# Performance work log

Hardware: AMD Instinct MI355X
Metric: run time of the kernel (lower is better)

The kernel has to match this reference:

```python
import jax, jax.numpy as jnp
import numpy as np

N = 50000      # nodes
E = 800000     # edges (before self-loops)
DIN = 146      # input feature dim
D = 128        # hidden/out dim
G = 64         # graphs in batch
L = 4          # number of GCNConv layers (len(hidden_dims[1:]) + 1)
NC = 10        # classes
EPS = 1e-5     # BatchNorm eps


def setup_inputs() -> dict:
    key = jax.random.key(0)
    ks = jax.random.split(key, 12)
    x = jax.random.normal(ks[0], (N, DIN), jnp.float32)
    edge_index = jax.random.randint(ks[1], (2, E), 0, N, dtype=jnp.int64)
    batch = jnp.sort(jax.random.randint(ks[2], (N,), 0, G, dtype=jnp.int64))

    def lin(k, shape, fan_in):
        return (jax.random.normal(k, shape, jnp.float32) / np.sqrt(fan_in)).astype(jnp.float32)

    W_emb = lin(ks[3], (DIN, D), DIN)
    b_emb = jnp.zeros((D,), jnp.float32)
    W_gcn = lin(ks[4], (L, D, D), D)
    b_gcn = jnp.zeros((L, D), jnp.float32)
    bn_gamma = jnp.ones((L, D), jnp.float32)
    bn_beta = jnp.zeros((L, D), jnp.float32)
    W_r1 = lin(ks[5], (D, D // 2), D)
    b_r1 = jnp.zeros((D // 2,), jnp.float32)
    W_r2 = lin(ks[6], (D // 2, D // 4), D // 2)
    b_r2 = jnp.zeros((D // 4,), jnp.float32)
    W_r3 = lin(ks[7], (D // 4, NC), D // 4)
    b_r3 = jnp.zeros((NC,), jnp.float32)
    return {"x": x, "edge_index": edge_index, "batch": batch,
            "W_emb": W_emb, "b_emb": b_emb, "W_gcn": W_gcn, "b_gcn": b_gcn,
            "bn_gamma": bn_gamma, "bn_beta": bn_beta,
            "W_r1": W_r1, "b_r1": b_r1, "W_r2": W_r2, "b_r2": b_r2,
            "W_r3": W_r3, "b_r3": b_r3}


def reference(x, edge_index, batch, W_emb, b_emb, W_gcn, b_gcn,
              bn_gamma, bn_beta, W_r1, b_r1, W_r2, b_r2, W_r3, b_r3):
    # gcn_norm with self-loops (fill_value=1, improved=False)
    loop = jnp.arange(N, dtype=edge_index.dtype)
    src = jnp.concatenate([edge_index[0], loop])
    dst = jnp.concatenate([edge_index[1], loop])
    deg = jax.ops.segment_sum(jnp.ones(src.shape, x.dtype), dst, num_segments=N)
    dinv = jax.lax.rsqrt(jnp.maximum(deg, jnp.asarray(1e-12, x.dtype)))  # deg >= 1 (self loops)
    norm = (dinv[src] * dinv[dst])[:, None]  # [E+N, 1]

    h = x @ W_emb + b_emb  # embedding_h
    for l in range(L):
        h_in = h
        m = h @ W_gcn[l]                                            # [N, D]
        h = jax.ops.segment_sum(m[src] * norm, dst, num_segments=N) + b_gcn[l]
        # BatchNorm1d (training-mode batch stats, biased var)
        mu = h.mean(axis=0)
        var = h.var(axis=0)
        h = (h - mu) * jax.lax.rsqrt(var + EPS) * bn_gamma[l] + bn_beta[l]
        h = jax.nn.relu(h)
        h = h_in + h  # residual (dims always match here)

    # global_mean_pool over batch ids
    sums = jax.ops.segment_sum(h, batch, num_segments=G)
    cnts = jax.ops.segment_sum(jnp.ones((N, 1), h.dtype), batch, num_segments=G)
    hg = sums / jnp.maximum(cnts, 1.0)

    # MLPReadout: two hidden layers halving dims, then classifier
    z = jax.nn.relu(hg @ W_r1 + b_r1)
    z = jax.nn.relu(z @ W_r2 + b_r2)
    return z @ W_r3 + b_r3  # [G, NC]
```

## Files before the change

kernel.cpp:

```cpp
#include <hip/hip_runtime.h>
#include <hip/hip_bf16.h>

#define NN 50000
#define EE 800000
#define DIN 146
#define DD 128
#define GG 64
#define LL 4
#define NC 10
#define BN_EPS 1e-5f

#define KP_EMB 160
#define AST_L  136
#define NCOPY 64
#define NPW 4
#define RST 129

#define C_INIT   256
#define C_REPACK (C_INIT + 31250)
#define C_BATCH  (C_REPACK + 196)
#define C_PARAMS (C_BATCH + 384)
#define C_WT     (C_PARAMS + 400)

#define B_GEMM 391
#define B_EDGE 782
#define B_TOT  (B_GEMM + B_EDGE)

typedef __attribute__((ext_vector_type(8))) short bf16x8;
typedef __attribute__((ext_vector_type(4))) float f32x4;

__device__ __forceinline__ float bf2f(__hip_bfloat16 v) { return __bfloat162float(v); }
__device__ __forceinline__ float loadf(const void* p, long i, int f32) {
    return f32 ? ((const float*)p)[i] : bf2f(((const __hip_bfloat16*)p)[i]);
}
__device__ __forceinline__ unsigned short f2bf_bits(float f) {
    __hip_bfloat16 h = __float2bfloat16(f);
    return *(unsigned short*)&h;
}
__device__ __forceinline__ float bfu2f(unsigned short u) {
    return __uint_as_float((unsigned)u << 16);
}
__device__ __forceinline__ void acc_add8(float* acc, uint4 v) {
    acc[0] += __uint_as_float(v.x << 16);
    acc[1] += __uint_as_float(v.x & 0xffff0000u);
    acc[2] += __uint_as_float(v.y << 16);
    acc[3] += __uint_as_float(v.y & 0xffff0000u);
    acc[4] += __uint_as_float(v.z << 16);
    acc[5] += __uint_as_float(v.z & 0xffff0000u);
    acc[6] += __uint_as_float(v.w << 16);
    acc[7] += __uint_as_float(v.w & 0xffff0000u);
}
__device__ __forceinline__ ushort4 pack4(f32x4 v) {
    ushort4 u;
    u.x = f2bf_bits(v[0]); u.y = f2bf_bits(v[1]);
    u.z = f2bf_bits(v[2]); u.w = f2bf_bits(v[3]);
    return u;
}
__device__ __forceinline__ ushort4 pack4s(f32x4 v, float s) {
    ushort4 u;
    u.x = f2bf_bits(s * v[0]); u.y = f2bf_bits(s * v[1]);
    u.z = f2bf_bits(s * v[2]); u.w = f2bf_bits(s * v[3]);
    return u;
}

__global__ void detect_kernel(const void* ei, const void* batch, const void* Wemb,
                              int* __restrict__ flags) {
    __shared__ int s_edge_nz, s_batch_nz, s_f32_cnt;
    int t = threadIdx.x;
    if (t == 0) { s_edge_nz = 0; s_batch_nz = 0; s_f32_cnt = 0; }
    __syncthreads();
    {   const int* w = (const int*)ei;
        long j = ((long)t * ((2L * EE) / 64)) | 1;
        if (w[j] != 0) atomicAdd(&s_edge_nz, 1);
    }
    {   const int* w = (const int*)batch;
        long j = ((long)(NN / 2) + (long)t * ((NN / 2) / 64)) | 1;
        if (j < NN && w[j] != 0) atomicAdd(&s_batch_nz, 1);
    }
    {   const unsigned short* w = (const unsigned short*)Wemb;
        unsigned short v = w[2 * t];
        int ex = (v >> 7) & 0xFF;
        if (v != 0 && ex >= 128) atomicAdd(&s_f32_cnt, 1);
    }
    __syncthreads();
    if (t == 0) {
        flags[0] = (s_edge_nz == 0) ? 1 : 0;
        flags[1] = (s_batch_nz == 0) ? 1 : 0;
        flags[2] = (s_f32_cnt >= 8) ? 1 : 0;
    }
}

struct Param { const void* src; float* dst; int src_n; int dst_n; };
struct Params12 { Param p[12]; };
struct WtDesc { const void* src; long src_off; unsigned short* dst; int K; int Kpad; };
struct WtDescs5 { WtDesc p[5]; };

__global__ __launch_bounds__(256) void mega_conv_kernel(
    const void* __restrict__ x, const void* __restrict__ batch,
    const int* __restrict__ flags, unsigned short* __restrict__ xb,
    int* __restrict__ deg, float* __restrict__ statmulti, float* __restrict__ hgsum,
    int* __restrict__ b32, Params12 P, WtDescs5 W)
{
    int b = blockIdx.x;
    int t = threadIdx.x;
    if (b < C_INIT) {
        int i = b * 256 + t;
        if (i < NN) deg[i] = 0;
        if (i < LL * NCOPY * 256) statmulti[i] = 0.0f;
        if (i < GG * DD) hgsum[i] = 0.0f;
    } else if (b < C_REPACK) {
        int f32 = flags[2];
        long idx = (long)(b - C_INIT) * 256 + t;
        int row = (int)(idx / KP_EMB);
        int k = (int)(idx - (long)row * KP_EMB);
        float v = (k < DIN) ? loadf(x, (long)row * DIN + k, f32) : 0.0f;
        xb[idx] = f2bf_bits(v);
    } else if (b < C_BATCH) {
        int i = (b - C_REPACK) * 256 + t;
        if (i < NN) b32[i] = flags[1] ? ((const int*)batch)[2L * i] : ((const int*)batch)[i];
    } else if (b < C_PARAMS) {
        int f32 = flags[2];
        int bb = b - C_BATCH;
        const Param& e = P.p[bb >> 5];
        int idx = (bb & 31) * 256 + t;
        if (idx < e.dst_n)
            e.dst[idx] = (idx < e.src_n) ? loadf(e.src, idx, f32) : 0.0f;
    } else {
        int f32 = flags[2];
        int bb = b - C_PARAMS;
        int y = bb / 80;
        const WtDesc& e = W.p[y];
        int idx = (bb - y * 80) * 256 + t;
        if (idx < 128 * e.Kpad) {
            int n = idx / e.Kpad, k = idx - n * e.Kpad;
            float v = (k < e.K) ? loadf(e.src, e.src_off + (long)k * DD + n, f32) : 0.0f;
            e.dst[idx] = f2bf_bits(v);
        }
    }
}


__global__ __launch_bounds__(256) void edge_emb_kernel(
    const void* __restrict__ ei, const int* __restrict__ flags,
    int* __restrict__ src32, int* __restrict__ dst32,
    int* __restrict__ rank, int* __restrict__ deg,
    const unsigned short* __restrict__ Ab,
    const unsigned short* __restrict__ Wt,
    const float* __restrict__ bias,
    unsigned short* __restrict__ hb, int n)
{
    int t = threadIdx.x;
    if (blockIdx.x >= B_GEMM) {
        int e0 = ((blockIdx.x - B_GEMM) * 256 + t) * 4;
        if (e0 >= EE) return;
        const int* w = (const int*)ei;
        int4 sv, dv;
        if (flags[0]) {
            int4 u0 = *(const int4*)(w + 2L * e0);
            int4 u1 = *(const int4*)(w + 2L * e0 + 4);
            int4 v0 = *(const int4*)(w + 2L * (EE + e0));
            int4 v1 = *(const int4*)(w + 2L * (EE + e0) + 4);
            sv = make_int4(u0.x, u0.z, u1.x, u1.z);
            dv = make_int4(v0.x, v0.z, v1.x, v1.z);
        } else {
            sv = *(const int4*)(w + e0);
            dv = *(const int4*)(w + EE + e0);
        }
        *(int4*)(src32 + e0) = sv;
        *(int4*)(dst32 + e0) = dv;
        int4 rv = make_int4(0, 0, 0, 0);
        if ((unsigned)dv.x < (unsigned)NN) rv.x = atomicAdd(&deg[dv.x], 1);
        if ((unsigned)dv.y < (unsigned)NN) rv.y = atomicAdd(&deg[dv.y], 1);
        if ((unsigned)dv.z < (unsigned)NN) rv.z = atomicAdd(&deg[dv.z], 1);
        if ((unsigned)dv.w < (unsigned)NN) rv.w = atomicAdd(&deg[dv.w], 1);
        *(int4*)(rank + e0) = rv;
        return;
    }
    int r0 = blockIdx.x * 128;
    int lane = t & 63, w = t >> 6;
    int m = lane & 15, quad = lane >> 4;
    int rbase = r0 + w * 32;
    bf16x8 a[2][5];
    #pragma unroll
    for (int rt = 0; rt < 2; ++rt)
        #pragma unroll
        for (int c = 0; c < 5; ++c) {
            int rr = rbase + rt * 16 + m; if (rr > n - 1) rr = n - 1;
            a[rt][c] = *(const bf16x8*)(Ab + (long)rr * KP_EMB + c * 32 + quad * 8);
        }
    f32x4 acc[2][8];
    #pragma unroll
    for (int t8 = 0; t8 < 8; ++t8) {
        float4 bv = *(const float4*)&bias[t8 * 16 + quad * 4];
        f32x4 ai = {bv.x, bv.y, bv.z, bv.w};
        acc[0][t8] = ai; acc[1][t8] = ai;
    }
    #pragma unroll
    for (int t8 = 0; t8 < 8; ++t8) {
        #pragma unroll
        for (int c = 0; c < 5; ++c) {
            bf16x8 b = *(const bf16x8*)(Wt + (long)(t8 * 16 + m) * KP_EMB + c * 32 + quad * 8);
            acc[0][t8] = __builtin_amdgcn_mfma_f32_16x16x32_bf16(b, a[0][c], acc[0][t8], 0, 0, 0);
            acc[1][t8] = __builtin_amdgcn_mfma_f32_16x16x32_bf16(b, a[1][c], acc[1][t8], 0, 0, 0);
        }
    }
    #pragma unroll
    for (int rt = 0; rt < 2; ++rt) {
        int row = rbase + rt * 16 + m;
        if (row < n) {
            #pragma unroll
            for (int t8 = 0; t8 < 8; ++t8)
                *(ushort4*)(hb + (long)row * DD + t8 * 16 + quad * 4) = pack4(acc[rt][t8]);
        }
    }
}

__global__ void scan1_kernel(const int* __restrict__ cnt, int* __restrict__ off,
                             int* __restrict__ bsum, float* __restrict__ dinv, int n) {
    int t = threadIdx.x;
    int i = blockIdx.x * 256 + t;
    int v = (i < n) ? cnt[i] : 0;
    if (i < n) dinv[i] = rsqrtf((float)(v + 1));
    int lane = t & 63, w = t >> 6;
    int x = v;
    #pragma unroll
    for (int s = 1; s < 64; s <<= 1) {
        int y = __shfl_up(x, s, 64);
        if (lane >= s) x += y;
    }
    __shared__ int wsum[4];
    if (lane == 63) wsum[w] = x;
    __syncthreads();
    if (t == 0) {
        int a = 0;
        #pragma unroll
        for (int k = 0; k < 4; ++k) { int tmp = wsum[k]; wsum[k] = a; a += tmp; }
        bsum[blockIdx.x] = a;
    }
    __syncthreads();
    int excl = x - v + wsum[w];
    if (i < n) off[i] = excl;
}

__global__ void scan2_kernel(int* __restrict__ bsum, int* __restrict__ boff,
                             int* __restrict__ off_last, int nb) {
    int t = threadIdx.x;
    int v = (t < nb) ? bsum[t] : 0;
    int lane = t & 63, w = t >> 6;
    int x = v;
    #pragma unroll
    for (int s = 1; s < 64; s <<= 1) {
        int y = __shfl_up(x, s, 64);
        if (lane >= s) x += y;
    }
    __shared__ int wsum[4];
    if (lane == 63) wsum[w] = x;
    __syncthreads();
    __shared__ int total_s;
    if (t == 0) {
        int a = 0;
        #pragma unroll
        for (int k = 0; k < 4; ++k) { int tmp = wsum[k]; wsum[k] = a; a += tmp; }
        total_s = a;
    }
    __syncthreads();
    int bval = x - v + wsum[w];
    if (t < nb) boff[t] = bval;
    if (t == nb - 1) *off_last = total_s - bval;
}

__global__ __launch_bounds__(256) void scat_mm_kernel(
    const int* __restrict__ src, const int* __restrict__ dst,
    const int* __restrict__ rank, const int* __restrict__ off,
    const int* __restrict__ boff, int* __restrict__ src_s,
    const unsigned short* __restrict__ Ab,
    const unsigned short* __restrict__ Wt,
    const float* __restrict__ dinv,
    unsigned short* __restrict__ Mb, int n)
{
    int t = threadIdx.x;
    if (blockIdx.x >= B_GEMM) {
        int e0 = ((blockIdx.x - B_GEMM) * 256 + t) * 4;
        if (e0 >= EE) return;
        int4 sv = *(const int4*)(src + e0);
        int4 dv = *(const int4*)(dst + e0);
        int4 rv = *(const int4*)(rank + e0);
        int ss[4] = {sv.x, sv.y, sv.z, sv.w};
        int dd2[4] = {dv.x, dv.y, dv.z, dv.w};
        int rr[4] = {rv.x, rv.y, rv.z, rv.w};
        int pos[4];
        #pragma unroll
        for (int k = 0; k < 4; ++k) {
            int d = dd2[k];
            int dcl = ((unsigned)d < (unsigned)NN) ? d : 0;
            pos[k] = off[dcl] + boff[dcl >> 8] + rr[k];
        }
        #pragma unroll
        for (int k = 0; k < 4; ++k)
            if ((unsigned)dd2[k] < (unsigned)NN && (unsigned)ss[k] < (unsigned)NN)
                src_s[pos[k]] = ss[k];
        return;
    }
    int r0 = blockIdx.x * 128;
    int lane = t & 63, w = t >> 6;
    int m = lane & 15, quad = lane >> 4;
    int rbase = r0 + w * 32;
    bf16x8 a[2][4];
    #pragma unroll
    for (int rt = 0; rt < 2; ++rt)
        #pragma unroll
        for (int c = 0; c < 4; ++c) {
            int rr = rbase + rt * 16 + m; if (rr > n - 1) rr = n - 1;
            a[rt][c] = *(const bf16x8*)(Ab + (long)rr * DD + c * 32 + quad * 8);
        }
    float dvt[2];
    int rowt[2];
    #pragma unroll
    for (int rt = 0; rt < 2; ++rt) {
        int rr = rbase + rt * 16 + m;
        rowt[rt] = rr;
        if (rr > n - 1) rr = n - 1;
        dvt[rt] = dinv[rr];
    }
    f32x4 acc[2][8];
    #pragma unroll
    for (int t8 = 0; t8 < 8; ++t8) {
        f32x4 z = {0.f, 0.f, 0.f, 0.f};
        acc[0][t8] = z; acc[1][t8] = z;
    }
    #pragma unroll
    for (int t8 = 0; t8 < 8; ++t8) {
        #pragma unroll
        for (int c = 0; c < 4; ++c) {
            bf16x8 b = *(const bf16x8*)(Wt + (long)(t8 * 16 + m) * DD + c * 32 + quad * 8);
            acc[0][t8] = __builtin_amdgcn_mfma_f32_16x16x32_bf16(b, a[0][c], acc[0][t8], 0, 0, 0);
            acc[1][t8] = __builtin_amdgcn_mfma_f32_16x16x32_bf16(b, a[1][c], acc[1][t8], 0, 0, 0);
        }
    }
    #pragma unroll
    for (int rt = 0; rt < 2; ++rt) {
        if (rowt[rt] < n) {
            #pragma unroll
            for (int t8 = 0; t8 < 8; ++t8)
                *(ushort4*)(Mb + (long)rowt[rt] * DD + t8 * 16 + quad * 4) = pack4s(acc[rt][t8], dvt[rt]);
        }
    }
}

__global__ __launch_bounds__(256) void gemm_fused_kernel(
    const unsigned short* __restrict__ aggb, unsigned short* __restrict__ hb,
    const float* __restrict__ statmulti, const float* __restrict__ gamma,
    const float* __restrict__ beta, const float* __restrict__ dinv,
    const unsigned short* __restrict__ Wt, unsigned short* __restrict__ Mb, int n)
{
    __shared__ unsigned short As[128 * AST_L];
    __shared__ float bnsh[256];
    int t = threadIdx.x;
    int r0 = blockIdx.x * 128;
    {
        float s = 0.0f;
        #pragma unroll 8
        for (int k = 0; k < NCOPY; ++k) s += statmulti[k * 256 + t];
        bnsh[t] = s;
    }
    __syncthreads();
    {
        int c4 = (t & 31) * 4, rsub = t >> 5;
        float inv_n = 1.0f / (float)n;
        float4 sm = *(const float4*)&bnsh[c4];
        float4 sq = *(const float4*)&bnsh[128 + c4];
        float4 ga = *(const float4*)&gamma[c4];
        float4 be = *(const float4*)&beta[c4];
        float4 mu, rs;
        mu.x = sm.x * inv_n; mu.y = sm.y * inv_n; mu.z = sm.z * inv_n; mu.w = sm.w * inv_n;
        rs.x = rsqrtf(sq.x * inv_n - mu.x * mu.x + BN_EPS) * ga.x;
        rs.y = rsqrtf(sq.y * inv_n - mu.y * mu.y + BN_EPS) * ga.y;
        rs.z = rsqrtf(sq.z * inv_n - mu.z * mu.z + BN_EPS) * ga.z;
        rs.w = rsqrtf(sq.w * inv_n - mu.w * mu.w + BN_EPS) * ga.w;
        #pragma unroll 4
        for (int i = 0; i < 16; ++i) {
            int row = i * 8 + rsub;
            int r = r0 + row;
            unsigned short o0 = 0, o1 = 0, o2 = 0, o3 = 0;
            if (r < n) {
                long g = (long)r * DD + c4;
                ushort4 au = *(const ushort4*)&aggb[g];
                ushort4 hu = *(const ushort4*)&hb[g];
                float h0 = bfu2f(hu.x) + fmaxf((bfu2f(au.x) - mu.x) * rs.x + be.x, 0.0f);
                float h1 = bfu2f(hu.y) + fmaxf((bfu2f(au.y) - mu.y) * rs.y + be.y, 0.0f);
                float h2 = bfu2f(hu.z) + fmaxf((bfu2f(au.z) - mu.z) * rs.z + be.z, 0.0f);
                float h3 = bfu2f(hu.w) + fmaxf((bfu2f(au.w) - mu.w) * rs.w + be.w, 0.0f);
                o0 = f2bf_bits(h0); o1 = f2bf_bits(h1);
                o2 = f2bf_bits(h2); o3 = f2bf_bits(h3);
                ushort4 ho; ho.x = o0; ho.y = o1; ho.z = o2; ho.w = o3;
                *(ushort4*)&hb[g] = ho;
            }
            unsigned short* dst = &As[row * AST_L + c4];
            dst[0] = o0; dst[1] = o1; dst[2] = o2; dst[3] = o3;
        }
    }
    __syncthreads();
    int lane = t & 63, w = t >> 6;
    int m = lane & 15, quad = lane >> 4;
    int rl = w * 32;
    int rbase = r0 + rl;
    bf16x8 a[2][4];
    #pragma unroll
    for (int rt = 0; rt < 2; ++rt)
        #pragma unroll
        for (int c = 0; c < 4; ++c)
            a[rt][c] = *(const bf16x8*)(As + (rl + rt * 16 + m) * AST_L + c * 32 + quad * 8);
    float dvt[2];
    int rowt[2];
    #pragma unroll
    for (int rt = 0; rt < 2; ++rt) {
        int rr = rbase + rt * 16 + m;
        rowt[rt] = rr;
        if (rr > n - 1) rr = n - 1;
        dvt[rt] = dinv[rr];
    }
    f32x4 acc[2][8];
    #pragma unroll
    for (int t8 = 0; t8 < 8; ++t8) {
        f32x4 z = {0.f, 0.f, 0.f, 0.f};
        acc[0][t8] = z; acc[1][t8] = z;
    }
    #pragma unroll
    for (int t8 = 0; t8 < 8; ++t8) {
        #pragma unroll
        for (int c = 0; c < 4; ++c) {
            bf16x8 b = *(const bf16x8*)(Wt + (long)(t8 * 16 + m) * DD + c * 32 + quad * 8);
            acc[0][t8] = __builtin_amdgcn_mfma_f32_16x16x32_bf16(b, a[0][c], acc[0][t8], 0, 0, 0);
            acc[1][t8] = __builtin_amdgcn_mfma_f32_16x16x32_bf16(b, a[1][c], acc[1][t8], 0, 0, 0);
        }
    }
    #pragma unroll
    for (int rt = 0; rt < 2; ++rt) {
        if (rowt[rt] < n) {
            #pragma unroll
            for (int t8 = 0; t8 < 8; ++t8)
                *(ushort4*)(Mb + (long)rowt[rt] * DD + t8 * 16 + quad * 4) = pack4s(acc[rt][t8], dvt[rt]);
        }
    }
}

__global__ __launch_bounds__(256) void agg_kernel(
    const unsigned short* __restrict__ mb, const int* __restrict__ off,
    const int* __restrict__ boff, const int* __restrict__ src_s,
    const float* __restrict__ dinv, const float* __restrict__ bias,
    unsigned short* __restrict__ aggb, float* __restrict__ statacc)
{
    __shared__ float sred[4][4 * RST];
    __shared__ float2 ssum[4][64], ssq[4][64];
    int t = threadIdx.x;
    int wv = t >> 6, lane = t & 63;
    int grp = lane >> 4, sl = lane & 15;
    float* red = sred[wv];
    float2 bi = ((const float2*)bias)[lane];
    float2 sAcc = {0.0f, 0.0f}, qAcc = {0.0f, 0.0f};
    int i0 = (blockIdx.x * 4 + wv) * NPW;
    #pragma unroll 1
    for (int ni = 0; ni < NPW; ++ni) {
        int i = i0 + ni;
        if (i >= NN) break;
        float acc[8];
        #pragma unroll
        for (int k = 0; k < 8; ++k) acc[k] = 0.0f;
        if (grp == 0) {
            uint4 v = *(const uint4*)(mb + (long)i * DD + sl * 8);
            acc_add8(acc, v);
        }
        int e  = off[i] + boff[i >> 8];
        int e1 = off[i + 1] + boff[(i + 1) >> 8];
        for (; e + 16 <= e1; e += 16) {
            int j0 = src_s[e + grp];
            int j1 = src_s[e + 4 + grp];
            int j2 = src_s[e + 8 + grp];
            int j3 = src_s[e + 12 + grp];
            uint4 v0 = *(const uint4*)(mb + (long)j0 * DD + sl * 8);
            uint4 v1 = *(const uint4*)(mb + (long)j1 * DD + sl * 8);
            uint4 v2 = *(const uint4*)(mb + (long)j2 * DD + sl * 8);
            uint4 v3 = *(const uint4*)(mb + (long)j3 * DD + sl * 8);
            acc_add8(acc, v0);
            acc_add8(acc, v1);
            acc_add8(acc, v2);
            acc_add8(acc, v3);
        }
        for (; e + 8 <= e1; e += 8) {
            int ja = src_s[e + grp];
            int jb = src_s[e + 4 + grp];
            uint4 va = *(const uint4*)(mb + (long)ja * DD + sl * 8);
            uint4 vb = *(const uint4*)(mb + (long)jb * DD + sl * 8);
            acc_add8(acc, va);
            acc_add8(acc, vb);
        }
        for (; e + 4 <= e1; e += 4) {
            int j = src_s[e + grp];
            uint4 v = *(const uint4*)(mb + (long)j * DD + sl * 8);
            acc_add8(acc, v);
        }
        if (e + grp < e1) {
            int j = src_s[e + grp];
            uint4 v = *(const uint4*)(mb + (long)j * DD + sl * 8);
            acc_add8(acc, v);
        }
        #pragma unroll
        for (int k = 0; k < 8; ++k) red[grp * RST + sl * 8 + k] = acc[k];
        asm volatile("" ::: "memory");
        float c0 = 0.0f, c1 = 0.0f;
        #pragma unroll
        for (int g = 0; g < 4; ++g) {
            c0 += red[g * RST + 2 * lane];
            c1 += red[g * RST + 2 * lane + 1];
        }
        asm volatile("" ::: "memory");
        float di = dinv[i];
        float o0 = di * c0 + bi.x;
        float o1 = di * c1 + bi.y;
        unsigned packed = ((unsigned)f2bf_bits(o1) << 16) | f2bf_bits(o0);
        ((unsigned*)aggb)[(long)i * 64 + lane] = packed;
        sAcc.x += o0; sAcc.y += o1;
        qAcc.x += o0 * o0; qAcc.y += o1 * o1;
    }
    ssum[wv][lane] = sAcc; ssq[wv][lane] = qAcc;
    __syncthreads();
    if (wv == 0) {
        float2 s0 = ssum[0][lane], s1 = ssum[1][lane], s2 = ssum[2][lane], s3 = ssum[3][lane];
        float2 q0 = ssq[0][lane], q1 = ssq[1][lane], q2 = ssq[2][lane], q3 = ssq[3][lane];
        float sx = s0.x + s1.x + s2.x + s3.x;
        float sy = s0.y + s1.y + s2.y + s3.y;
        float qx = q0.x + q1.x + q2.x + q3.x;
        float qy = q0.y + q1.y + q2.y + q3.y;
        float* copy = statacc + (blockIdx.x & (NCOPY - 1)) * 256;
        atomicAdd(&copy[2 * lane], sx);
        atomicAdd(&copy[2 * lane + 1], sy);
        atomicAdd(&copy[128 + 2 * lane], qx);
        atomicAdd(&copy[128 + 2 * lane + 1], qy);
    }
}

__global__ void pool1_kernel(const unsigned short* __restrict__ hb,
                             const unsigned short* __restrict__ aggb,
                             const float* __restrict__ statmulti,
                             const float* __restrict__ gamma, const float* __restrict__ beta,
                             const int* __restrict__ b32, float* __restrict__ hgsum, int n) {
    __shared__ float bnsh[256];
    int t = threadIdx.x;
    {
        float s = 0.0f;
        #pragma unroll 8
        for (int k = 0; k < NCOPY; ++k) s += statmulti[k * 256 + t];
        bnsh[t] = s;
    }
    __syncthreads();
    int c4 = (t & 31) * 4, rsub = t >> 5;
    float inv_n = 1.0f / (float)n;
    float4 sm = *(const float4*)&bnsh[c4];
    float4 sq = *(const float4*)&bnsh[128 + c4];
    float4 ga = *(const float4*)&gamma[c4];
    float4 be = *(const float4*)&beta[c4];
    float4 mu, rs;
    mu.x = sm.x * inv_n; mu.y = sm.y * inv_n; mu.z = sm.z * inv_n; mu.w = sm.w * inv_n;
    rs.x = rsqrtf(sq.x * inv_n - mu.x * mu.x + BN_EPS) * ga.x;
    rs.y = rsqrtf(sq.y * inv_n - mu.y * mu.y + BN_EPS) * ga.y;
    rs.z = rsqrtf(sq.z * inv_n - mu.z * mu.z + BN_EPS) * ga.z;
    rs.w = rsqrtf(sq.w * inv_n - mu.w * mu.w + BN_EPS) * ga.w;
    int rows_pb = (n + gridDim.x - 1) / gridDim.x;
    int r0 = blockIdx.x * rows_pb;
    int r1 = min(n, r0 + rows_pb);
    float4 acc = {0, 0, 0, 0};
    int gcur = -1;
    for (int r = r0 + rsub; r < r1; r += 8) {
        int g = b32[r];
        if (g != gcur) {
            if (gcur >= 0) {
                atomicAdd(&hgsum[gcur * DD + c4 + 0], acc.x);
                atomicAdd(&hgsum[gcur * DD + c4 + 1], acc.y);
                atomicAdd(&hgsum[gcur * DD + c4 + 2], acc.z);
                atomicAdd(&hgsum[gcur * DD + c4 + 3], acc.w);
            }
            acc.x = acc.y = acc.z = acc.w = 0.0f;
            gcur = ((unsigned)g < (unsigned)GG) ? g : -1;
        }
        if (gcur >= 0) {
            long ix = (long)r * DD + c4;
            ushort4 au = *(const ushort4*)&aggb[ix];
            ushort4 hu = *(const ushort4*)&hb[ix];
            acc.x += bfu2f(hu.x) + fmaxf((bfu2f(au.x) - mu.x) * rs.x + be.x, 0.0f);
            acc.y += bfu2f(hu.y) + fmaxf((bfu2f(au.y) - mu.y) * rs.y + be.y, 0.0f);
            acc.z += bfu2f(hu.z) + fmaxf((bfu2f(au.z) - mu.z) * rs.z + be.z, 0.0f);
            acc.w += bfu2f(hu.w) + fmaxf((bfu2f(au.w) - mu.w) * rs.w + be.w, 0.0f);
        }
    }
    if (gcur >= 0) {
        atomicAdd(&hgsum[gcur * DD + c4 + 0], acc.x);
        atomicAdd(&hgsum[gcur * DD + c4 + 1], acc.y);
        atomicAdd(&hgsum[gcur * DD + c4 + 2], acc.z);
        atomicAdd(&hgsum[gcur * DD + c4 + 3], acc.w);
    }
}

__device__ int lower_bound_i(const int* __restrict__ a, int n, int v) {
    int lo = 0, hi = n;
    while (lo < hi) {
        int mid = (lo + hi) >> 1;
        if (a[mid] < v) lo = mid + 1; else hi = mid;
    }
    return lo;
}

__global__ void readout_kernel(const float* __restrict__ hgsum, const int* __restrict__ b32,
                               const float* __restrict__ W1, const float* __restrict__ b1,
                               const float* __restrict__ W2, const float* __restrict__ b2,
                               const float* __restrict__ W3, const float* __restrict__ b3,
                               const int* __restrict__ flags, void* __restrict__ out, int n) {
    int f32 = flags[2];
    int g = blockIdx.x;
    int t = threadIdx.x;
    __shared__ float hgs[DD];
    __shared__ float z1[DD / 2];
    __shared__ float z2[DD / 4];
    int lo = lower_bound_i(b32, n, g);
    int hi = lower_bound_i(b32, n, g + 1);
    float invc = 1.0f / fmaxf((float)(hi - lo), 1.0f);
    hgs[t] = hgsum[g * DD + t] * invc;
    __syncthreads();
    if (t < DD / 2) {
        float acc = b1[t];
        #pragma unroll 8
        for (int k = 0; k < DD; ++k) acc = fmaf(hgs[k], W1[k * (DD / 2) + t], acc);
        z1[t] = fmaxf(acc, 0.0f);
    }
    __syncthreads();
    if (t < DD / 4) {
        float acc = b2[t];
        #pragma unroll 8
        for (int k = 0; k < DD / 2; ++k) acc = fmaf(z1[k], W2[k * (DD / 4) + t], acc);
        z2[t] = fmaxf(acc, 0.0f);
    }
    __syncthreads();
    if (t < NC) {
        float acc = b3[t];
        #pragma unroll 8
        for (int k = 0; k < DD / 4; ++k) acc = fmaf(z2[k], W3[k * NC + t], acc);
        if (f32) ((float*)out)[g * NC + t] = acc;
        else     ((__hip_bfloat16*)out)[g * NC + t] = __float2bfloat16(acc);
    }
}

extern "C" void kernel_launch(void* const* d_in, const int* in_sizes, int n_in,
                              void* d_out, int out_size, void* d_ws, size_t ws_size,
                              hipStream_t stream) {
    const void* x      = d_in[0];
    const void* ei     = d_in[1];
    const void* batch  = d_in[2];
    const void* W_emb  = d_in[3];
    const void* b_emb  = d_in[4];
    const void* W_gcn  = d_in[5];
    const void* b_gcn  = d_in[6];
    const void* bn_g   = d_in[7];
    const void* bn_b   = d_in[8];
    const void* W_r1   = d_in[9];
    const void* b_r1   = d_in[10];
    const void* W_r2   = d_in[11];
    const void* b_r2   = d_in[12];
    const void* W_r3   = d_in[13];
    const void* b_r3   = d_in[14];

    char* p = (char*)d_ws;
    auto alloc = [&](size_t bytes) -> void* {
        void* r = (void*)p;
        p += (bytes + 255) & ~(size_t)255;
        return r;
    };
    int*   flags  = (int*)alloc(64 * 4);
    int*   deg    = (int*)alloc((size_t)NN * 4);
    float* statmulti = (float*)alloc((size_t)LL * NCOPY * 256 * 4);
    float* hgsum  = (float*)alloc((size_t)GG * DD * 4);
    int*   off    = (int*)alloc((size_t)(NN + 1) * 4);
    float* dinv   = (float*)alloc((size_t)NN * 4);
    int*   src32  = (int*)alloc((size_t)EE * 4);
    int*   dst32  = (int*)alloc((size_t)EE * 4);
    int*   rank   = (int*)alloc((size_t)EE * 4);
    int*   b32    = (int*)alloc((size_t)NN * 4);
    int*   src_s  = (int*)alloc((size_t)EE * 4);
    int*   bsum   = (int*)alloc(256 * 4);
    int*   boff   = (int*)alloc(256 * 4);
    unsigned short* hb = (unsigned short*)alloc((size_t)NN * DD * 2);
    unsigned short* mb = (unsigned short*)alloc((size_t)NN * DD * 2);
    unsigned short* aggb = (unsigned short*)alloc((size_t)NN * DD * 2);
    unsigned short* xb = (unsigned short*)alloc((size_t)NN * KP_EMB * 2);
    unsigned short* wt_emb = (unsigned short*)alloc((size_t)DD * KP_EMB * 2);
    unsigned short* wt_gcn = (unsigned short*)alloc((size_t)LL * DD * DD * 2);
    float* b_emb32 = (float*)alloc(DD * 4);
    float* b_gcn32 = (float*)alloc((size_t)LL * DD * 4);
    float* bng32   = (float*)alloc((size_t)LL * DD * 4);
    float* bnb32   = (float*)alloc((size_t)LL * DD * 4);
    float* wr1     = (float*)alloc((size_t)DD * (DD / 2) * 4);
    float* br1     = (float*)alloc((DD / 2) * 4);
    float* wr2     = (float*)alloc((size_t)(DD / 2) * (DD / 4) * 4);
    float* br2     = (float*)alloc((DD / 4) * 4);
    float* wr3     = (float*)alloc((size_t)(DD / 4) * NC * 4);
    float* br3     = (float*)alloc(NC * 4);

    detect_kernel<<<1, 64, 0, stream>>>(ei, batch, W_emb, flags);

    Params12 P;
    P.p[0]  = { b_emb, b_emb32, DD, DD };
    P.p[1]  = { b_gcn, b_gcn32, LL * DD, LL * DD };
    P.p[2]  = { bn_g,  bng32,   LL * DD, LL * DD };
    P.p[3]  = { bn_b,  bnb32,   LL * DD, LL * DD };
    P.p[4]  = { W_r1,  wr1,     DD * (DD / 2), DD * (DD / 2) };
    P.p[5]  = { b_r1,  br1,     DD / 2, DD / 2 };
    P.p[6]  = { W_r2,  wr2,     (DD / 2) * (DD / 4), (DD / 2) * (DD / 4) };
    P.p[7]  = { b_r2,  br2,     DD / 4, DD / 4 };
    P.p[8]  = { W_r3,  wr3,     (DD / 4) * NC, (DD / 4) * NC };
    P.p[9]  = { b_r3,  br3,     NC, NC };
    P.p[10] = { b_r3,  br3,     0, 0 };
    P.p[11] = { b_r3,  br3,     0, 0 };

    WtDescs5 W;
    W.p[0] = { W_emb, 0,            wt_emb,                DIN, KP_EMB };
    W.p[1] = { W_gcn, 0L * DD * DD, wt_gcn + 0L * DD * DD, DD,  DD };
    W.p[2] = { W_gcn, 1L * DD * DD, wt_gcn + 1L * DD * DD, DD,  DD };
    W.p[3] = { W_gcn, 2L * DD * DD, wt_gcn + 2L * DD * DD, DD,  DD };
    W.p[4] = { W_gcn, 3L * DD * DD, wt_gcn + 3L * DD * DD, DD,  DD };

    mega_conv_kernel<<<C_WT, 256, 0, stream>>>(x, batch, flags, xb, deg, statmulti,
                                               hgsum, b32, P, W);

    edge_emb_kernel<<<B_TOT, 256, 0, stream>>>(ei, flags, src32, dst32, rank, deg,
                                               xb, wt_emb, b_emb32, hb, NN);

    int nb = (NN + 255) / 256;
    scan1_kernel<<<nb, 256, 0, stream>>>(deg, off, bsum, dinv, NN);
    scan2_kernel<<<1, 256, 0, stream>>>(bsum, boff, off + NN, nb);

    scat_mm_kernel<<<B_TOT, 256, 0, stream>>>(src32, dst32, rank, off, boff, src_s,
                                              hb, wt_gcn, dinv, mb, NN);

    int ngemm = (NN + 127) / 128;
    int nagg = (NN + 4 * NPW - 1) / (4 * NPW);
    for (int l = 0; l < LL; ++l) {
        if (l > 0) {
            gemm_fused_kernel<<<ngemm, 256, 0, stream>>>(
                aggb, hb, statmulti + (size_t)(l - 1) * NCOPY * 256,
                bng32 + (l - 1) * DD, bnb32 + (l - 1) * DD,
                dinv, wt_gcn + (size_t)l * DD * DD, mb, NN);
        }
        agg_kernel<<<nagg, 256, 0, stream>>>(mb, off, boff, src_s, dinv,
                                             b_gcn32 + l * DD, aggb,
                                             statmulti + (size_t)l * NCOPY * 256);
    }

    pool1_kernel<<<512, 256, 0, stream>>>(hb, aggb, statmulti + (size_t)(LL - 1) * NCOPY * 256,
                                          bng32 + (LL - 1) * DD, bnb32 + (LL - 1) * DD,
                                          b32, hgsum, NN);
    readout_kernel<<<GG, DD, 0, stream>>>(hgsum, b32, wr1, br1, wr2, br2, wr3, br3,
                                          flags, d_out, NN);
}
```

Baseline: 429.0 us.

## Replace global-atomic CSR build with two-level bucketed counting sort

Rebuilds the CSR construction as a two-pass bucket sort. Edges are packed (src<<8 | dst&255), histogrammed into 196 buckets of 256 destinations using shared-memory atomics, scanned per bucket, scattered into bucket order, and then each bucket is sorted locally in shared memory to produce offsets, dinv and src_s. This removes the 800K global atomicAdds on the degree array and the random scatter over the whole edge range. The cost is more kernel launches, extra intermediate buffers, and the first-layer GEMM now runs as its own kernel instead of overlapping with the scatter.

```diff
diff --git a/kernel.cpp b/kernel.cpp
--- a/kernel.cpp
+++ b/kernel.cpp
@@ -16,15 +16,19 @@
 #define NPW 4
 #define RST 129
 
-#define C_INIT   256
-#define C_REPACK (C_INIT + 31250)
-#define C_BATCH  (C_REPACK + 196)
-#define C_PARAMS (C_BATCH + 384)
-#define C_WT     (C_PARAMS + 400)
+#define NBKT 196
+#define BHP  200
+#define NBE  782
+
+#define A_EDGE   NBE
+#define A_INIT   (A_EDGE + 256)
+#define A_REPACK (A_INIT + 31250)
+#define A_BATCH  (A_REPACK + 196)
+#define A_PARAMS (A_BATCH + 384)
+#define A_WT     (A_PARAMS + 400)
 
 #define B_GEMM 391
-#define B_EDGE 782
-#define B_TOT  (B_GEMM + B_EDGE)
+#define C_TOT  (B_GEMM + NBE)
 
 typedef __attribute__((ext_vector_type(8))) short bf16x8;
 typedef __attribute__((ext_vector_type(4))) float f32x4;
@@ -63,6 +67,27 @@
     return u;
 }
 
+__device__ __forceinline__ int blk_excl_scan(int v, int t, int* wsum, int* total_sh) {
+    __syncthreads();
+    int lane = t & 63, w = t >> 6;
+    int x = v;
+    #pragma unroll
+    for (int s = 1; s < 64; s <<= 1) {
+        int y = __shfl_up(x, s, 64);
+        if (lane >= s) x += y;
+    }
+    if (lane == 63) wsum[w] = x;
+    __syncthreads();
+    if (t == 0) {
+        int a = 0;
+        #pragma unroll
+        for (int k = 0; k < 4; ++k) { int tmp = wsum[k]; wsum[k] = a; a += tmp; }
+        *total_sh = a;
+    }
+    __syncthreads();
+    return x - v + wsum[w];
+}
+
 __global__ void detect_kernel(const void* ei, const void* batch, const void* Wemb,
                               int* __restrict__ flags) {
     __shared__ int s_edge_nz, s_batch_nz, s_f32_cnt;
@@ -96,38 +121,75 @@
 struct WtDescs5 { WtDesc p[5]; };
 
 __global__ __launch_bounds__(256) void mega_conv_kernel(
-    const void* __restrict__ x, const void* __restrict__ batch,
-    const int* __restrict__ flags, unsigned short* __restrict__ xb,
-    int* __restrict__ deg, float* __restrict__ statmulti, float* __restrict__ hgsum,
-    int* __restrict__ b32, Params12 P, WtDescs5 W)
+    const void* __restrict__ x, const void* __restrict__ ei,
+    const void* __restrict__ batch, const int* __restrict__ flags,
+    unsigned short* __restrict__ xb, float* __restrict__ statmulti,
+    float* __restrict__ hgsum, int* __restrict__ b32,
+    unsigned* __restrict__ pk, unsigned char* __restrict__ bkt,
+    int* __restrict__ bh, Params12 P, WtDescs5 W)
 {
     int b = blockIdx.x;
     int t = threadIdx.x;
-    if (b < C_INIT) {
-        int i = b * 256 + t;
-        if (i < NN) deg[i] = 0;
+    if (b < A_EDGE) {
+        __shared__ int hist[NBKT];
+        if (t < NBKT) hist[t] = 0;
+        __syncthreads();
+        int e0 = (b * 256 + t) * 4;
+        if (e0 < EE) {
+            const int* w = (const int*)ei;
+            int4 sv, dv;
+            if (flags[0]) {
+                int4 u0 = *(const int4*)(w + 2L * e0);
+                int4 u1 = *(const int4*)(w + 2L * e0 + 4);
+                int4 v0 = *(const int4*)(w + 2L * (EE + e0));
+                int4 v1 = *(const int4*)(w + 2L * (EE + e0) + 4);
+                sv = make_int4(u0.x, u0.z, u1.x, u1.z);
+                dv = make_int4(v0.x, v0.z, v1.x, v1.z);
+            } else {
+                sv = *(const int4*)(w + e0);
+                dv = *(const int4*)(w + EE + e0);
+            }
+            int ss[4] = {sv.x, sv.y, sv.z, sv.w};
+            int dd2[4] = {dv.x, dv.y, dv.z, dv.w};
+            unsigned pk4[4], bk4[4];
+            #pragma unroll
+            for (int k = 0; k < 4; ++k) {
+                unsigned s = min((unsigned)ss[k], (unsigned)(NN - 1));
+                unsigned d = min((unsigned)dd2[k], (unsigned)(NN - 1));
+                pk4[k] = (s << 8) | (d & 255u);
+                bk4[k] = d >> 8;
+                atomicAdd(&hist[bk4[k]], 1);
+            }
+            *(uint4*)(pk + e0) = make_uint4(pk4[0], pk4[1], pk4[2], pk4[3]);
+            *(uchar4*)(bkt + e0) = make_uchar4((unsigned char)bk4[0], (unsigned char)bk4[1],
+                                               (unsigned char)bk4[2], (unsigned char)bk4[3]);
+        }
+        __syncthreads();
+        if (t < NBKT) bh[b * BHP + t] = hist[t];
+    } else if (b < A_INIT) {
+        int i = (b - A_EDGE) * 256 + t;
         if (i < LL * NCOPY * 256) statmulti[i] = 0.0f;
         if (i < GG * DD) hgsum[i] = 0.0f;
-    } else if (b < C_REPACK) {
+    } else if (b < A_REPACK) {
         int f32 = flags[2];
-        long idx = (long)(b - C_INIT) * 256 + t;
+        long idx = (long)(b - A_INIT) * 256 + t;
         int row = (int)(idx / KP_EMB);
         int k = (int)(idx - (long)row * KP_EMB);
         float v = (k < DIN) ? loadf(x, (long)row * DIN + k, f32) : 0.0f;
         xb[idx] = f2bf_bits(v);
-    } else if (b < C_BATCH) {
-        int i = (b - C_REPACK) * 256 + t;
+    } else if (b < A_BATCH) {
+        int i = (b - A_REPACK) * 256 + t;
         if (i < NN) b32[i] = flags[1] ? ((const int*)batch)[2L * i] : ((const int*)batch)[i];
-    } else if (b < C_PARAMS) {
+    } else if (b < A_PARAMS) {
         int f32 = flags[2];
-        int bb = b - C_BATCH;
+        int bb = b - A_BATCH;
         const Param& e = P.p[bb >> 5];
         int idx = (bb & 31) * 256 + t;
         if (idx < e.dst_n)
             e.dst[idx] = (idx < e.src_n) ? loadf(e.src, idx, f32) : 0.0f;
     } else {
         int f32 = flags[2];
-        int bb = b - C_PARAMS;
+        int bb = b - A_PARAMS;
         int y = bb / 80;
         const WtDesc& e = W.p[y];
         int idx = (bb - y * 80) * 256 + t;
@@ -139,11 +201,37 @@
     }
 }
 
-
-__global__ __launch_bounds__(256) void edge_emb_kernel(
-    const void* __restrict__ ei, const int* __restrict__ flags,
-    int* __restrict__ src32, int* __restrict__ dst32,
-    int* __restrict__ rank, int* __restrict__ deg,
+__global__ __launch_bounds__(256) void bscan_kernel(int* __restrict__ bh, int* __restrict__ tot) {
+    __shared__ int wsum[4], total_sh;
+    int b = blockIdx.x;
+    int t = threadIdx.x;
+    int carry = 0;
+    #pragma unroll 1
+    for (int c = 0; c < 4; ++c) {
+        int i = c * 256 + t;
+        int v = (i < NBE) ? bh[i * BHP + b] : 0;
+        int excl = blk_excl_scan(v, t, wsum, &total_sh);
+        if (i < NBE) bh[i * BHP + b] = excl + carry;
+        carry += total_sh;
+    }
+    if (t == 0) tot[b] = carry;
+}
+
+__global__ void bscan2_kernel(const int* __restrict__ tot, int* __restrict__ base,
+                              int* __restrict__ off_last) {
+    __shared__ int wsum[4], total_sh;
+    int t = threadIdx.x;
+    int v = (t < NBKT) ? tot[t] : 0;
+    int excl = blk_excl_scan(v, t, wsum, &total_sh);
+    if (t < NBKT) base[t] = excl;
+    if (t == 0) { base[NBKT] = total_sh; *off_last = total_sh; }
+}
+
+
+__global__ __launch_bounds__(256) void bucket_emb_kernel(
+    const unsigned* __restrict__ pk, const unsigned char* __restrict__ bkt,
+    const int* __restrict__ bh, const int* __restrict__ base,
+    unsigned* __restrict__ bucketA,
     const unsigned short* __restrict__ Ab,
     const unsigned short* __restrict__ Wt,
     const float* __restrict__ bias,
@@ -151,29 +239,22 @@
 {
     int t = threadIdx.x;
     if (blockIdx.x >= B_GEMM) {
-        int e0 = ((blockIdx.x - B_GEMM) * 256 + t) * 4;
-        if (e0 >= EE) return;
-        const int* w = (const int*)ei;
-        int4 sv, dv;
-        if (flags[0]) {
-            int4 u0 = *(const int4*)(w + 2L * e0);
-            int4 u1 = *(const int4*)(w + 2L * e0 + 4);
-            int4 v0 = *(const int4*)(w + 2L * (EE + e0));
-            int4 v1 = *(const int4*)(w + 2L * (EE + e0) + 4);
-            sv = make_int4(u0.x, u0.z, u1.x, u1.z);
-            dv = make_int4(v0.x, v0.z, v1.x, v1.z);
-        } else {
-            sv = *(const int4*)(w + e0);
-            dv = *(const int4*)(w + EE + e0);
-        }
-        *(int4*)(src32 + e0) = sv;
-        *(int4*)(dst32 + e0) = dv;
-        int4 rv = make_int4(0, 0, 0, 0);
-        if ((unsigned)dv.x < (unsigned)NN) rv.x = atomicAdd(&deg[dv.x], 1);
-        if ((unsigned)dv.y < (unsigned)NN) rv.y = atomicAdd(&deg[dv.y], 1);
-        if ((unsigned)dv.z < (unsigned)NN) rv.z = atomicAdd(&deg[dv.z], 1);
-        if ((unsigned)dv.w < (unsigned)NN) rv.w = atomicAdd(&deg[dv.w], 1);
-        *(int4*)(rank + e0) = rv;
+        int bb = blockIdx.x - B_GEMM;
+        __shared__ int cur[NBKT];
+        if (t < NBKT) cur[t] = bh[bb * BHP + t] + base[t];
+        __syncthreads();
+        int e0 = (bb * 256 + t) * 4;
+        if (e0 < EE) {
+            uint4 p4 = *(const uint4*)(pk + e0);
+            uchar4 b4 = *(const uchar4*)(bkt + e0);
+            unsigned pks[4] = {p4.x, p4.y, p4.z, p4.w};
+            unsigned bks[4] = {b4.x, b4.y, b4.z, b4.w};
+            #pragma unroll
+            for (int k = 0; k < 4; ++k) {
+                int slot = atomicAdd(&cur[bks[k]], 1);
+                bucketA[slot] = pks[k];
+            }
+        }
         return;
     }
     int r0 = blockIdx.x * 128;
@@ -215,92 +296,41 @@
     }
 }
 
-__global__ void scan1_kernel(const int* __restrict__ cnt, int* __restrict__ off,
-                             int* __restrict__ bsum, float* __restrict__ dinv, int n) {
-    int t = threadIdx.x;
-    int i = blockIdx.x * 256 + t;
-    int v = (i < n) ? cnt[i] : 0;
-    if (i < n) dinv[i] = rsqrtf((float)(v + 1));
-    int lane = t & 63, w = t >> 6;
-    int x = v;
-    #pragma unroll
-    for (int s = 1; s < 64; s <<= 1) {
-        int y = __shfl_up(x, s, 64);
-        if (lane >= s) x += y;
-    }
-    __shared__ int wsum[4];
-    if (lane == 63) wsum[w] = x;
-    __syncthreads();
-    if (t == 0) {
-        int a = 0;
-        #pragma unroll
-        for (int k = 0; k < 4; ++k) { int tmp = wsum[k]; wsum[k] = a; a += tmp; }
-        bsum[blockIdx.x] = a;
-    }
-    __syncthreads();
-    int excl = x - v + wsum[w];
-    if (i < n) off[i] = excl;
-}
-
-__global__ void scan2_kernel(int* __restrict__ bsum, int* __restrict__ boff,
-                             int* __restrict__ off_last, int nb) {
-    int t = threadIdx.x;
-    int v = (t < nb) ? bsum[t] : 0;
-    int lane = t & 63, w = t >> 6;
-    int x = v;
-    #pragma unroll
-    for (int s = 1; s < 64; s <<= 1) {
-        int y = __shfl_up(x, s, 64);
-        if (lane >= s) x += y;
-    }
-    __shared__ int wsum[4];
-    if (lane == 63) wsum[w] = x;
-    __syncthreads();
-    __shared__ int total_s;
-    if (t == 0) {
-        int a = 0;
-        #pragma unroll
-        for (int k = 0; k < 4; ++k) { int tmp = wsum[k]; wsum[k] = a; a += tmp; }
-        total_s = a;
-    }
-    __syncthreads();
-    int bval = x - v + wsum[w];
-    if (t < nb) boff[t] = bval;
-    if (t == nb - 1) *off_last = total_s - bval;
-}
-
-__global__ __launch_bounds__(256) void scat_mm_kernel(
-    const int* __restrict__ src, const int* __restrict__ dst,
-    const int* __restrict__ rank, const int* __restrict__ off,
-    const int* __restrict__ boff, int* __restrict__ src_s,
+__global__ __launch_bounds__(256) void csr_kernel(
+    const unsigned* __restrict__ bucketA, const int* __restrict__ base,
+    int* __restrict__ off, float* __restrict__ dinv, int* __restrict__ src_s)
+{
+    __shared__ int dg[256], cur[256], wsum[4], total_sh;
+    int b = blockIdx.x, t = threadIdx.x;
+    int eb0 = base[b], eb1 = base[b + 1];
+    dg[t] = 0;
+    __syncthreads();
+    for (int e = eb0 + t; e < eb1; e += 256)
+        atomicAdd(&dg[bucketA[e] & 255u], 1);
+    __syncthreads();
+    int v = dg[t];
+    int excl = blk_excl_scan(v, t, wsum, &total_sh);
+    int node = b * 256 + t;
+    if (node < NN) {
+        off[node] = eb0 + excl;
+        dinv[node] = rsqrtf((float)(v + 1));
+    }
+    cur[t] = excl;
+    __syncthreads();
+    for (int e = eb0 + t; e < eb1; e += 256) {
+        unsigned pv = bucketA[e];
+        int r = atomicAdd(&cur[pv & 255u], 1);
+        src_s[eb0 + r] = (int)(pv >> 8);
+    }
+}
+
+__global__ __launch_bounds__(256) void gemm_plain_kernel(
     const unsigned short* __restrict__ Ab,
     const unsigned short* __restrict__ Wt,
     const float* __restrict__ dinv,
     unsigned short* __restrict__ Mb, int n)
 {
     int t = threadIdx.x;
-    if (blockIdx.x >= B_GEMM) {
-        int e0 = ((blockIdx.x - B_GEMM) * 256 + t) * 4;
-        if (e0 >= EE) return;
-        int4 sv = *(const int4*)(src + e0);
-        int4 dv = *(const int4*)(dst + e0);
-        int4 rv = *(const int4*)(rank + e0);
-        int ss[4] = {sv.x, sv.y, sv.z, sv.w};
-        int dd2[4] = {dv.x, dv.y, dv.z, dv.w};
-        int rr[4] = {rv.x, rv.y, rv.z, rv.w};
-        int pos[4];
-        #pragma unroll
-        for (int k = 0; k < 4; ++k) {
-            int d = dd2[k];
-            int dcl = ((unsigned)d < (unsigned)NN) ? d : 0;
-            pos[k] = off[dcl] + boff[dcl >> 8] + rr[k];
-        }
-        #pragma unroll
-        for (int k = 0; k < 4; ++k)
-            if ((unsigned)dd2[k] < (unsigned)NN && (unsigned)ss[k] < (unsigned)NN)
-                src_s[pos[k]] = ss[k];
-        return;
-    }
     int r0 = blockIdx.x * 128;
     int lane = t & 63, w = t >> 6;
     int m = lane & 15, quad = lane >> 4;
@@ -446,7 +476,7 @@
 
 __global__ __launch_bounds__(256) void agg_kernel(
     const unsigned short* __restrict__ mb, const int* __restrict__ off,
-    const int* __restrict__ boff, const int* __restrict__ src_s,
+    const int* __restrict__ src_s,
     const float* __restrict__ dinv, const float* __restrict__ bias,
     unsigned short* __restrict__ aggb, float* __restrict__ statacc)
 {
@@ -470,8 +500,8 @@
             uint4 v = *(const uint4*)(mb + (long)i * DD + sl * 8);
             acc_add8(acc, v);
         }
-        int e  = off[i] + boff[i >> 8];
-        int e1 = off[i + 1] + boff[(i + 1) >> 8];
+        int e  = off[i];
+        int e1 = off[i + 1];
         for (; e + 16 <= e1; e += 16) {
             int j0 = src_s[e + grp];
             int j1 = src_s[e + 4 + grp];
@@ -674,18 +704,18 @@
         return r;
     };
     int*   flags  = (int*)alloc(64 * 4);
-    int*   deg    = (int*)alloc((size_t)NN * 4);
     float* statmulti = (float*)alloc((size_t)LL * NCOPY * 256 * 4);
     float* hgsum  = (float*)alloc((size_t)GG * DD * 4);
     int*   off    = (int*)alloc((size_t)(NN + 1) * 4);
     float* dinv   = (float*)alloc((size_t)NN * 4);
-    int*   src32  = (int*)alloc((size_t)EE * 4);
-    int*   dst32  = (int*)alloc((size_t)EE * 4);
-    int*   rank   = (int*)alloc((size_t)EE * 4);
     int*   b32    = (int*)alloc((size_t)NN * 4);
     int*   src_s  = (int*)alloc((size_t)EE * 4);
-    int*   bsum   = (int*)alloc(256 * 4);
-    int*   boff   = (int*)alloc(256 * 4);
+    unsigned* pk  = (unsigned*)alloc((size_t)EE * 4);
+    unsigned char* bkt = (unsigned char*)alloc((size_t)EE);
+    int*   bh     = (int*)alloc((size_t)NBE * BHP * 4);
+    int*   tot    = (int*)alloc(256 * 4);
+    int*   base   = (int*)alloc(256 * 4);
+    unsigned* bucketA = (unsigned*)alloc((size_t)EE * 4);
     unsigned short* hb = (unsigned short*)alloc((size_t)NN * DD * 2);
     unsigned short* mb = (unsigned short*)alloc((size_t)NN * DD * 2);
     unsigned short* aggb = (unsigned short*)alloc((size_t)NN * DD * 2);
@@ -726,18 +756,18 @@
     W.p[3] = { W_gcn, 2L * DD * DD, wt_gcn + 2L * DD * DD, DD,  DD };
     W.p[4] = { W_gcn, 3L * DD * DD, wt_gcn + 3L * DD * DD, DD,  DD };
 
-    mega_conv_kernel<<<C_WT, 256, 0, stream>>>(x, batch, flags, xb, deg, statmulti,
-                                               hgsum, b32, P, W);
-
-    edge_emb_kernel<<<B_TOT, 256, 0, stream>>>(ei, flags, src32, dst32, rank, deg,
-                                               xb, wt_emb, b_emb32, hb, NN);
-
-    int nb = (NN + 255) / 256;
-    scan1_kernel<<<nb, 256, 0, stream>>>(deg, off, bsum, dinv, NN);
-    scan2_kernel<<<1, 256, 0, stream>>>(bsum, boff, off + NN, nb);
-
-    scat_mm_kernel<<<B_TOT, 256, 0, stream>>>(src32, dst32, rank, off, boff, src_s,
-                                              hb, wt_gcn, dinv, mb, NN);
+    mega_conv_kernel<<<A_WT, 256, 0, stream>>>(x, ei, batch, flags, xb, statmulti,
+                                               hgsum, b32, pk, bkt, bh, P, W);
+
+    bscan_kernel<<<NBKT, 256, 0, stream>>>(bh, tot);
+    bscan2_kernel<<<1, 256, 0, stream>>>(tot, base, off + NN);
+
+    bucket_emb_kernel<<<C_TOT, 256, 0, stream>>>(pk, bkt, bh, base, bucketA,
+                                                 xb, wt_emb, b_emb32, hb, NN);
+
+    csr_kernel<<<NBKT, 256, 0, stream>>>(bucketA, base, off, dinv, src_s);
+
+    gemm_plain_kernel<<<(NN + 127) / 128, 256, 0, stream>>>(hb, wt_gcn, dinv, mb, NN);
 
     int ngemm = (NN + 127) / 128;
     int nagg = (NN + 4 * NPW - 1) / (4 * NPW);
@@ -748,7 +778,7 @@
                 bng32 + (l - 1) * DD, bnb32 + (l - 1) * DD,
                 dinv, wt_gcn + (size_t)l * DD * DD, mb, NN);
         }
-        agg_kernel<<<nagg, 256, 0, stream>>>(mb, off, boff, src_s, dinv,
+        agg_kernel<<<nagg, 256, 0, stream>>>(mb, off, src_s, dinv,
                                              b_gcn32 + l * DD, aggb,
                                              statmulti + (size_t)l * NCOPY * 256);
     }
```

Result: faster. 413.3 us (-3.6%).
